# Kernel optimization log

Measured on AMD Instinct MI355X. Metric: run time of the kernel, lower is better.

The kernel has to match this reference:

```python
import jax, jax.numpy as jnp
import numpy as np

MAX_FRAMES = 12
EMBED_DIM = 512
TOPK = 12
NUM_SAMPLES = 500
SIGMA = 0.05
SEL_DIM = 2
NUM_HEADS = 2


def setup_inputs() -> dict:
    key = jax.random.key(0)
    ks = jax.random.split(key, 9)
    D = EMBED_DIM
    C = D // 2
    s = lambda fan_in: 1.0 / np.sqrt(fan_in)
    return {
        "x": jax.random.normal(ks[0], (16, MAX_FRAMES * 50, D), dtype=jnp.float32),
        "ln_g": jnp.ones((D,), jnp.float32),
        "ln_b": jnp.zeros((D,), jnp.float32),
        "w_in": jax.random.normal(ks[1], (D, C), jnp.float32) * s(D),
        "wq": jax.random.normal(ks[2], (C, C), jnp.float32) * s(C),
        "wk": jax.random.normal(ks[3], (C, C), jnp.float32) * s(C),
        "wv": jax.random.normal(ks[4], (C, C), jnp.float32) * s(C),
        "wo": jax.random.normal(ks[5], (C, C), jnp.float32) * s(C),
        "w1": jax.random.normal(ks[6], (2 * C, C), jnp.float32) * s(2 * C),
        "w2": jax.random.normal(ks[7], (C, 1), jnp.float32) * s(C),
    }


def layer_norm(x, g, b, eps=1e-5):
    mu = jnp.mean(x, axis=-1, keepdims=True)
    var = jnp.var(x, axis=-1, keepdims=True)
    return (x - mu) * jax.lax.rsqrt(var + eps) * g + b


def mha(x, wq, wk, wv, wo):
    B, N, C = x.shape
    hd = C // NUM_HEADS
    q = (x @ wq).reshape(B, N, NUM_HEADS, hd).transpose(0, 2, 1, 3)
    k = (x @ wk).reshape(B, N, NUM_HEADS, hd).transpose(0, 2, 1, 3)
    v = (x @ wv).reshape(B, N, NUM_HEADS, hd).transpose(0, 2, 1, 3)
    attn = jax.nn.softmax(jnp.einsum('bhnd,bhmd->bhnm', q, k) / np.sqrt(hd), axis=-1)
    out = jnp.einsum('bhnm,bhmd->bhnd', attn, v).transpose(0, 2, 1, 3).reshape(B, N, C)
    return out @ wo


def predictor(x, ln_g, ln_b, w_in, wq, wk, wv, wo, w1, w2):
    h = jax.nn.gelu(layer_norm(x, ln_g, ln_b) @ w_in, approximate=False)
    h = mha(h, wq, wk, wv, wo)
    B, N, C = h.shape
    g = jnp.mean(h, axis=1, keepdims=True)
    h = jnp.concatenate([h, jnp.broadcast_to(g, (B, N, C))], axis=-1)
    h = jax.nn.gelu(h @ w1, approximate=False)
    return jnp.tanh(h @ w2)  # (B, N, 1)


def perturbed_topk(scores):
    # scores: (b, d) -> soft indicators (b, k, d)
    b, d = scores.shape
    noise = jax.random.normal(jax.random.key(1), (b, NUM_SAMPLES, d), dtype=scores.dtype)
    perturbed = scores[:, None, :] + noise * SIGMA
    _, idx = jax.lax.top_k(perturbed, TOPK)            # (b, ns, k)
    idx = jnp.sort(idx, axis=-1)
    onehot = jax.nn.one_hot(idx, d, dtype=scores.dtype)  # (b, ns, k, d)
    return onehot.mean(axis=1)                          # (b, k, d)


def reference(x, ln_g, ln_b, w_in, wq, wk, wv, wo, w1, w2):
    B, L, D = x.shape
    N = L // MAX_FRAMES
    xf = x.reshape(B * MAX_FRAMES, N, D)
    pred = predictor(xf, ln_g, ln_b, w_in, wq, wk, wv, wo, w1, w2)[..., 0]  # (b, N)
    spatial_score = pred[:, SEL_DIM:]                    # (b, N-2)
    ind = perturbed_topk(spatial_score)                  # (b, k, N-2)
    cls_feat = xf[:, :SEL_DIM, :]
    spatial_feat = xf[:, SEL_DIM:, :]
    sel = jnp.einsum('bkl,bld->bkd', ind, spatial_feat)
    out = jnp.concatenate([cls_feat, sel], axis=1)       # (b, 2+k, D)
    return out.reshape(B, -1, D)
```

## Files before the change

kernel.cpp:

```cpp
#include <hip/hip_runtime.h>
#include <stdint.h>

#define B2      192
#define NTOK    50
#define ROWS    9600
#define D_EMB   512
#define C_DIM   256
#define HD      128
#define NSAMP   500
#define TOPKK   12
#define NSPA    48
#define NSAMP_T 96000
#define NOISE_OFF 61953536ull
#define NOISE_BYTES 18432000ull
#define WS_NEED (NOISE_OFF + NOISE_BYTES)

typedef short short8 __attribute__((ext_vector_type(8)));
typedef float f32x4  __attribute__((ext_vector_type(4)));

__device__ __forceinline__ float gelu_f(float x) {
    return 0.5f * x * (1.0f + erff(x * 0.7071067811865476f));
}
__device__ __forceinline__ uint16_t f2bf(float x) {
    uint32_t u = __float_as_uint(x);
    return (uint16_t)((u + 0x7fffu + ((u >> 16) & 1u)) >> 16);
}
__device__ __forceinline__ float bf2f(uint16_t b) {
    return __uint_as_float(((uint32_t)b) << 16);
}
__device__ __forceinline__ size_t swzA(int m, int k, int K) {
    return ((size_t)(m >> 4) * (K >> 5) + (k >> 5)) * 512
         + (size_t)((((k >> 3) & 3) * 16 + (m & 15)) * 8 + (k & 7));
}

__device__ __forceinline__ uint32_t rotl32(uint32_t x, int r) {
    return (x << r) | (x >> (32 - r));
}
__device__ __forceinline__ void threefry01(uint32_t& x0, uint32_t& x1) {
    const uint32_t ks0 = 0u, ks1 = 1u, ks2 = 0x1BD11BDBu;
    x0 += ks0; x1 += ks1;
#define TFR(r) { x0 += x1; x1 = rotl32(x1, r); x1 ^= x0; }
    TFR(13) TFR(15) TFR(26) TFR(6)  x0 += ks1; x1 += ks2 + 1u;
    TFR(17) TFR(29) TFR(16) TFR(24) x0 += ks2; x1 += ks0 + 2u;
    TFR(13) TFR(15) TFR(26) TFR(6)  x0 += ks0; x1 += ks1 + 3u;
    TFR(17) TFR(29) TFR(16) TFR(24) x0 += ks1; x1 += ks2 + 4u;
    TFR(13) TFR(15) TFR(26) TFR(6)  x0 += ks2; x1 += ks0 + 5u;
#undef TFR
}

__device__ __forceinline__ float erfinv_xla(float x) {
    float w = -log1pf(-x * x);
    float p;
    if (w < 5.0f) {
        w -= 2.5f;
        p = 2.81022636e-08f;
        p = fmaf(p, w, 3.43273939e-07f);
        p = fmaf(p, w, -3.5233877e-06f);
        p = fmaf(p, w, -4.39150654e-06f);
        p = fmaf(p, w, 0.00021858087f);
        p = fmaf(p, w, -0.00125372503f);
        p = fmaf(p, w, -0.00417768164f);
        p = fmaf(p, w, 0.246640727f);
        p = fmaf(p, w, 1.50140941f);
    } else {
        w = sqrtf(w) - 3.0f;
        p = -0.000200214257f;
        p = fmaf(p, w, 0.000100950558f);
        p = fmaf(p, w, 0.00134934322f);
        p = fmaf(p, w, -0.00367342844f);
        p = fmaf(p, w, 0.00573950773f);
        p = fmaf(p, w, -0.0076224613f);
        p = fmaf(p, w, 0.00943887047f);
        p = fmaf(p, w, 1.00167406f);
        p = fmaf(p, w, 2.83297682f);
    }
    return p * x;
}

__device__ __forceinline__ float bits_to_normal(uint32_t bits) {
    float f = __uint_as_float((bits >> 9) | 0x3f800000u) - 1.0f;
    float u = f * 2.0f + (-0.99999994039535522461f);
    u = fmaxf(-0.99999994039535522461f, u);
    return 1.4142135623730951f * erfinv_xla(u);
}

__global__ __launch_bounds__(256) void noise_kernel(float* __restrict__ noise) {
    int T  = blockIdx.x * 256 + threadIdx.x;
    int q  = T / NSAMP_T;
    int g2 = T - q * NSAMP_T;
    uint32_t cbase = (uint32_t)g2 * 48u + (uint32_t)(q * 4);
    float4 o;
    { uint32_t x0=0u, x1=cbase + 0u; threefry01(x0,x1); o.x = bits_to_normal(x0^x1) * 0.05f; }
    { uint32_t x0=0u, x1=cbase + 1u; threefry01(x0,x1); o.y = bits_to_normal(x0^x1) * 0.05f; }
    { uint32_t x0=0u, x1=cbase + 2u; threefry01(x0,x1); o.z = bits_to_normal(x0^x1) * 0.05f; }
    { uint32_t x0=0u, x1=cbase + 3u; threefry01(x0,x1); o.w = bits_to_normal(x0^x1) * 0.05f; }
    ((float4*)noise)[(size_t)q * NSAMP_T + g2] = o;
}

__global__ __launch_bounds__(256) void prep_kernel(const float* __restrict__ x,
                                                   const float* __restrict__ g,
                                                   const float* __restrict__ b,
                                                   short* __restrict__ xh,
                                                   short* __restrict__ xl,
                                                   const float* __restrict__ w_in, const float* __restrict__ wq,
                                                   const float* __restrict__ wk, const float* __restrict__ wv,
                                                   const float* __restrict__ wo, const float* __restrict__ w1,
                                                   short* win_hi, short* win_lo, short* wq_hi, short* wq_lo,
                                                   short* wk_hi, short* wk_lo, short* wv_hi, short* wv_lo,
                                                   short* wo_hi, short* wo_lo, short* w1a_hi, short* w1a_lo) {
    if (blockIdx.x < 2400) {
        int row  = blockIdx.x * 4 + (threadIdx.x >> 6);
        int lane = threadIdx.x & 63;
        const float* rp = x + (size_t)row * D_EMB;
        float4 v0 = *(const float4*)(rp + lane * 8);
        float4 v1 = *(const float4*)(rp + lane * 8 + 4);
        float s  = v0.x + v0.y + v0.z + v0.w + v1.x + v1.y + v1.z + v1.w;
        float s2 = v0.x*v0.x + v0.y*v0.y + v0.z*v0.z + v0.w*v0.w
                 + v1.x*v1.x + v1.y*v1.y + v1.z*v1.z + v1.w*v1.w;
#pragma unroll
        for (int off = 32; off; off >>= 1) {
            s  += __shfl_xor(s,  off);
            s2 += __shfl_xor(s2, off);
        }
        float mu  = s / 512.0f;
        float var = s2 / 512.0f - mu * mu;
        float inv = 1.0f / sqrtf(var + 1e-5f);
        const float* gp = g + lane * 8;
        const float* bp = b + lane * 8;
        float o[8];
        o[0]=(v0.x-mu)*inv*gp[0]+bp[0]; o[1]=(v0.y-mu)*inv*gp[1]+bp[1];
        o[2]=(v0.z-mu)*inv*gp[2]+bp[2]; o[3]=(v0.w-mu)*inv*gp[3]+bp[3];
        o[4]=(v1.x-mu)*inv*gp[4]+bp[4]; o[5]=(v1.y-mu)*inv*gp[5]+bp[5];
        o[6]=(v1.z-mu)*inv*gp[6]+bp[6]; o[7]=(v1.w-mu)*inv*gp[7]+bp[7];
        short8 h8, l8;
#pragma unroll
        for (int j = 0; j < 8; ++j) {
            uint16_t h = f2bf(o[j]);
            h8[j] = (short)h;
            l8[j] = (short)f2bf(o[j] - bf2f(h));
        }
        size_t blk = (size_t)(row >> 4) * 16 + (lane >> 2);
        int inner  = (lane & 3) * 16 + (row & 15);
        ((short8*)xh)[blk * 64 + inner] = h8;
        ((short8*)xl)[blk * 64 + inner] = l8;
    } else {
        int blk = blockIdx.x - 2400;
        const float* W; short *hi, *lo; int K, base;
        if      (blk <  64) { W = w_in; hi = win_hi; lo = win_lo; K = 512; base = 0;   }
        else if (blk <  96) { W = wq;   hi = wq_hi;  lo = wq_lo;  K = 256; base = 64;  }
        else if (blk < 128) { W = wk;   hi = wk_hi;  lo = wk_lo;  K = 256; base = 96;  }
        else if (blk < 160) { W = wv;   hi = wv_hi;  lo = wv_lo;  K = 256; base = 128; }
        else if (blk < 192) { W = wo;   hi = wo_hi;  lo = wo_lo;  K = 256; base = 160; }
        else                { W = w1;   hi = w1a_hi; lo = w1a_lo; K = 256; base = 192; }
        int t = (blk - base) * 256 + threadIdx.x;
        int n = t & 255, k8 = t >> 8;
        short8 h8, l8;
#pragma unroll
        for (int j = 0; j < 8; ++j) {
            float wvl = W[(size_t)(k8 * 8 + j) * 256 + n];
            uint16_t h = f2bf(wvl);
            h8[j] = (short)h;
            l8[j] = (short)f2bf(wvl - bf2f(h));
        }
        size_t bb = (size_t)(n >> 4) * (K >> 5) + (k8 >> 2);
        int inner = (k8 & 3) * 16 + (n & 15);
        ((short8*)hi)[bb * 64 + inner] = h8;
        ((short8*)lo)[bb * 64 + inner] = l8;
    }
}

template<int KB>
__device__ __forceinline__ void mm_core(const short8* __restrict__ pAh, const short8* __restrict__ pAl,
                                        const short8* __restrict__ pBh0, const short8* __restrict__ pBl0,
                                        const short8* __restrict__ pBh1, const short8* __restrict__ pBl1,
                                        f32x4& acc0, f32x4& acc1) {
    short8 ah[3], al[3], bh0[3], bl0[3], bh1[3], bl1[3];
#pragma unroll
    for (int i = 0; i < 2; ++i) {
        int off = i * 64;
        ah[i] = pAh[off];  al[i] = pAl[off];
        bh0[i] = pBh0[off]; bl0[i] = pBl0[off];
        bh1[i] = pBh1[off]; bl1[i] = pBl1[off];
    }
#pragma unroll
    for (int ks = 0; ks < KB; ++ks) {
        int cur = ks % 3;
        if (ks + 2 < KB) {
            int pre = (ks + 2) % 3, off = (ks + 2) * 64;
            ah[pre] = pAh[off];  al[pre] = pAl[off];
            bh0[pre] = pBh0[off]; bl0[pre] = pBl0[off];
            bh1[pre] = pBh1[off]; bl1[pre] = pBl1[off];
        }
        acc0 = __builtin_amdgcn_mfma_f32_16x16x32_bf16(ah[cur], bh0[cur], acc0, 0, 0, 0);
        acc0 = __builtin_amdgcn_mfma_f32_16x16x32_bf16(ah[cur], bl0[cur], acc0, 0, 0, 0);
        acc0 = __builtin_amdgcn_mfma_f32_16x16x32_bf16(al[cur], bh0[cur], acc0, 0, 0, 0);
        acc1 = __builtin_amdgcn_mfma_f32_16x16x32_bf16(ah[cur], bh1[cur], acc1, 0, 0, 0);
        acc1 = __builtin_amdgcn_mfma_f32_16x16x32_bf16(ah[cur], bl1[cur], acc1, 0, 0, 0);
        acc1 = __builtin_amdgcn_mfma_f32_16x16x32_bf16(al[cur], bh1[cur], acc1, 0, 0, 0);
    }
}

__device__ __forceinline__ void epi_store(f32x4 acc, int row0, int col, int N,
                                          float* __restrict__ Cf, short* __restrict__ Chi,
                                          short* __restrict__ Clo,
                                          const float* __restrict__ bias, int act) {
#pragma unroll
    for (int r = 0; r < 4; ++r) {
        int row = row0 + r;
        float v2 = acc[r];
        if (bias) v2 += bias[(size_t)(row / 50) * N + col];
        if (act)  v2 = gelu_f(v2);
        if (Cf) Cf[(size_t)row * N + col] = v2;
        if (Chi) {
            uint16_t h = f2bf(v2);
            size_t ad = swzA(row, col, 256);
            Chi[ad] = (short)h;
            Clo[ad] = (short)f2bf(v2 - bf2f(h));
        }
    }
}

template<int KB>
__global__ __launch_bounds__(256) void gemm_one(const short8* __restrict__ Ah,
                                                const short8* __restrict__ Al,
                                                const short8* __restrict__ Bh,
                                                const short8* __restrict__ Bl,
                                                float* __restrict__ Cf,
                                                short* __restrict__ Chi,
                                                short* __restrict__ Clo,
                                                const float* __restrict__ bias,
                                                int act) {
    int lane = threadIdx.x & 63;
    int wv   = threadIdx.x >> 6;
    int ms   = blockIdx.x * 4 + wv;
    int ns0  = blockIdx.y * 2;
    const short8* pAh  = Ah + (size_t)ms  * KB * 64 + lane;
    const short8* pAl  = Al + (size_t)ms  * KB * 64 + lane;
    const short8* pBh0 = Bh + (size_t)ns0 * KB * 64 + lane;
    const short8* pBl0 = Bl + (size_t)ns0 * KB * 64 + lane;
    const short8* pBh1 = pBh0 + (size_t)KB * 64;
    const short8* pBl1 = pBl0 + (size_t)KB * 64;
    f32x4 acc0 = {0.f,0.f,0.f,0.f}, acc1 = {0.f,0.f,0.f,0.f};
    mm_core<KB>(pAh, pAl, pBh0, pBl0, pBh1, pBl1, acc0, acc1);
    int row0 = ms * 16 + (lane >> 4) * 4;
    int cin  = lane & 15;
    epi_store(acc0, row0, ns0 * 16 + cin,      256, Cf, Chi, Clo, bias, act);
    epi_store(acc1, row0, (ns0 + 1) * 16 + cin, 256, Cf, Chi, Clo, bias, act);
}

__global__ __launch_bounds__(256) void gemm8_pred(const short8* __restrict__ Ah,
                                                  const short8* __restrict__ Al,
                                                  const short8* __restrict__ Bh,
                                                  const short8* __restrict__ Bl,
                                                  const float* __restrict__ gwb,
                                                  const float* __restrict__ w2,
                                                  float* __restrict__ pred_raw) {
    int lane = threadIdx.x & 63;
    int wv   = threadIdx.x >> 6;
    int ms   = blockIdx.x * 4 + wv;
    int ns0  = blockIdx.y * 2;
    const short8* pAh  = Ah + (size_t)ms  * 8 * 64 + lane;
    const short8* pAl  = Al + (size_t)ms  * 8 * 64 + lane;
    const short8* pBh0 = Bh + (size_t)ns0 * 8 * 64 + lane;
    const short8* pBl0 = Bl + (size_t)ns0 * 8 * 64 + lane;
    const short8* pBh1 = pBh0 + 8 * 64;
    const short8* pBl1 = pBl0 + 8 * 64;
    f32x4 acc0 = {0.f,0.f,0.f,0.f}, acc1 = {0.f,0.f,0.f,0.f};
    mm_core<8>(pAh, pAl, pBh0, pBl0, pBh1, pBl1, acc0, acc1);
    int row0 = ms * 16 + (lane >> 4) * 4;
    int cin  = lane & 15;
    int c0   = ns0 * 16 + cin;
    int c1   = (ns0 + 1) * 16 + cin;
    float w2a = w2[c0], w2b = w2[c1];
#pragma unroll
    for (int r = 0; r < 4; ++r) {
        int row = row0 + r;
        int bb  = row / 50;
        float v0 = gelu_f(acc0[r] + gwb[(size_t)bb * 256 + c0]);
        float v1 = gelu_f(acc1[r] + gwb[(size_t)bb * 256 + c1]);
        float t  = v0 * w2a + v1 * w2b;
        t += __shfl_xor(t, 1); t += __shfl_xor(t, 2);
        t += __shfl_xor(t, 4); t += __shfl_xor(t, 8);
        if (cin == 0) atomicAdd(&pred_raw[row], t);
    }
}

__global__ __launch_bounds__(256) void gemm_qkv(const short8* __restrict__ Ah,
                                                const short8* __restrict__ Al,
                                                const short8* __restrict__ Bhq, const short8* __restrict__ Blq,
                                                const short8* __restrict__ Bhk, const short8* __restrict__ Blk,
                                                const short8* __restrict__ Bhv, const short8* __restrict__ Blv,
                                                float* __restrict__ q, float* __restrict__ k,
                                                float* __restrict__ v) {
    int lane = threadIdx.x & 63;
    int wv   = threadIdx.x >> 6;
    int ms   = blockIdx.x * 4 + wv;
    int sel  = blockIdx.y >> 3;
    int ns0  = (blockIdx.y & 7) * 2;
    const short8* Bh = (sel == 0) ? Bhq : (sel == 1) ? Bhk : Bhv;
    const short8* Bl = (sel == 0) ? Blq : (sel == 1) ? Blk : Blv;
    float* C = (sel == 0) ? q : (sel == 1) ? k : v;
    const short8* pAh  = Ah + (size_t)ms  * 8 * 64 + lane;
    const short8* pAl  = Al + (size_t)ms  * 8 * 64 + lane;
    const short8* pBh0 = Bh + (size_t)ns0 * 8 * 64 + lane;
    const short8* pBl0 = Bl + (size_t)ns0 * 8 * 64 + lane;
    const short8* pBh1 = pBh0 + 8 * 64;
    const short8* pBl1 = pBl0 + 8 * 64;
    f32x4 acc0 = {0.f,0.f,0.f,0.f}, acc1 = {0.f,0.f,0.f,0.f};
    mm_core<8>(pAh, pAl, pBh0, pBl0, pBh1, pBl1, acc0, acc1);
    int row0 = ms * 16 + (lane >> 4) * 4;
    int cin  = lane & 15;
    epi_store(acc0, row0, ns0 * 16 + cin,      256, C, nullptr, nullptr, nullptr, 0);
    epi_store(acc1, row0, (ns0 + 1) * 16 + cin, 256, C, nullptr, nullptr, nullptr, 0);
}

#define ASLOT(r, s) ((r) * 128 + (((s) ^ (((r) >> 2) & 7)) << 2))
__global__ __launch_bounds__(256) void attn_kernel(const float* __restrict__ q,
                                                   const float* __restrict__ k,
                                                   const float* __restrict__ v,
                                                   short* __restrict__ aoh,
                                                   short* __restrict__ aol) {
    __shared__ float sQ[NTOK * 128];
    __shared__ float sK[NTOK * 128];
    __shared__ float sS[NTOK * 51];
    int blk = blockIdx.x;
    int b = blk >> 1, h = blk & 1;
    const size_t base = (size_t)b * NTOK * C_DIM + h * HD;
    int tid = threadIdx.x;
    for (int idx = tid; idx < 1600; idx += 256) {
        int r = idx >> 5, s = idx & 31;
        int ps = ASLOT(r, s);
        *(float4*)&sQ[ps] = *(const float4*)(q + base + (size_t)r * C_DIM + s * 4);
        *(float4*)&sK[ps] = *(const float4*)(k + base + (size_t)r * C_DIM + s * 4);
    }
    __syncthreads();
    if (tid < 169) {
        int i2 = tid / 13, j2 = tid - i2 * 13;
        int i0 = i2 * 4, j0 = j2 * 4;
        int kq = i2 & 7, kk = j2 & 7;
        const float* qp[4];
        const float* kp[4];
#pragma unroll
        for (int r = 0; r < 4; ++r) {
            int ir = i0 + r; if (ir > 49) ir = 49;
            int jr = j0 + r; if (jr > 49) jr = 49;
            qp[r] = &sQ[ir * 128];
            kp[r] = &sK[jr * 128];
        }
        f32x4 acc[4][4];
#pragma unroll
        for (int r = 0; r < 4; ++r)
#pragma unroll
            for (int c = 0; c < 4; ++c) acc[r][c] = (f32x4){0.f, 0.f, 0.f, 0.f};
#pragma unroll 4
        for (int t = 0; t < 32; ++t) {
            int oq = (t ^ kq) << 2, ok = (t ^ kk) << 2;
            f32x4 qr[4], kr[4];
#pragma unroll
            for (int r = 0; r < 4; ++r) qr[r] = *(const f32x4*)(qp[r] + oq);
#pragma unroll
            for (int c = 0; c < 4; ++c) kr[c] = *(const f32x4*)(kp[c] + ok);
#pragma unroll
            for (int r = 0; r < 4; ++r)
#pragma unroll
                for (int c = 0; c < 4; ++c) acc[r][c] += qr[r] * kr[c];
        }
        const float sc = 0.08838834764831845f;
#pragma unroll
        for (int r = 0; r < 4; ++r) {
            if (i0 + r < 50) {
#pragma unroll
                for (int c = 0; c < 4; ++c) {
                    if (j0 + c < 50) {
                        f32x4 a = acc[r][c];
                        sS[(i0 + r) * 51 + (j0 + c)] = (a[0] + a[1] + a[2] + a[3]) * sc;
                    }
                }
            }
        }
    }
    __syncthreads();
    for (int idx = tid; idx < 1600; idx += 256) {
        int r = idx >> 5, s = idx & 31;
        *(float4*)&sQ[ASLOT(r, s)] = *(const float4*)(v + base + (size_t)r * C_DIM + s * 4);
    }
    {
        int wid = tid >> 6, lane = tid & 63;
        for (int i = wid; i < NTOK; i += 4) {
            float val = (lane < NTOK) ? sS[i * 51 + lane] : -3.0e38f;
            float m = val;
#pragma unroll
            for (int off = 32; off; off >>= 1) m = fmaxf(m, __shfl_xor(m, off));
            float e2 = expf(val - m);
            float s = e2;
#pragma unroll
            for (int off = 32; off; off >>= 1) s += __shfl_xor(s, off);
            if (lane < NTOK) sS[i * 51 + lane] = e2 * (1.0f / s);
        }
    }
    __syncthreads();
    for (int e = tid; e < 416; e += 256) {
        int i2 = e >> 5;
        int s4 = e & 31;
        int i0 = i2 * 4;
        const float* sr[4];
#pragma unroll
        for (int r = 0; r < 4; ++r) {
            int ir = i0 + r; if (ir > 49) ir = 49;
            sr[r] = &sS[ir * 51];
        }
        f32x4 acc[4];
#pragma unroll
        for (int r = 0; r < 4; ++r) acc[r] = (f32x4){0.f, 0.f, 0.f, 0.f};
        for (int j = 0; j < NTOK; ++j) {
            f32x4 v4 = *(const f32x4*)&sQ[ASLOT(j, s4)];
#pragma unroll
            for (int r = 0; r < 4; ++r) acc[r] += v4 * sr[r][j];
        }
#pragma unroll
        for (int r = 0; r < 4; ++r) {
            if (i0 + r < 50) {
                int row = b * NTOK + i0 + r;
#pragma unroll
                for (int c = 0; c < 4; ++c) {
                    int col = h * HD + s4 * 4 + c;
                    float val = acc[r][c];
                    uint16_t hh2 = f2bf(val);
                    size_t ad = swzA(row, col, 256);
                    aoh[ad] = (short)hh2;
                    aol[ad] = (short)f2bf(val - bf2f(hh2));
                }
            }
        }
    }
}
#undef ASLOT

__global__ __launch_bounds__(256) void mean_gw(const float* __restrict__ h2,
                                               const float* __restrict__ w1,
                                               float* __restrict__ gw) {
    __shared__ float sg[C_DIM];
    int b = blockIdx.x, d = threadIdx.x;
    float s = 0.f;
    for (int n = 0; n < NTOK; ++n) s += h2[((size_t)b * NTOK + n) * C_DIM + d];
    sg[d] = s * 0.02f;
    __syncthreads();
    const float* wb = w1 + 256 * 256;
    float acc = 0.f;
#pragma unroll 4
    for (int k = 0; k < C_DIM; ++k)
        acc = fmaf(sg[k], wb[(size_t)k * 256 + d], acc);
    gw[(size_t)b * C_DIM + d] = acc;
}

__device__ __forceinline__ unsigned long long topk_key(uint32_t base, int d,
                                                       const float* __restrict__ sp) {
    uint32_t x0 = 0u, x1 = base + (uint32_t)d;
    threefry01(x0, x1);
    float n  = bits_to_normal(x0 ^ x1);
    float v  = tanhf(sp[d]) + n * 0.05f;
    uint32_t vb   = __float_as_uint(v);
    uint32_t mono = (vb & 0x80000000u) ? ~vb : (vb | 0x80000000u);
    return ((unsigned long long)mono << 6) | (unsigned)(63 - d);
}

#define STEP(li) { unsigned long long mn_ = (key < li) ? key : li; \
                   li = (key > li) ? key : li; key = mn_; }
#define S1  STEP(l0)
#define S2  S1  STEP(l1)
#define S3  S2  STEP(l2)
#define S4  S3  STEP(l3)
#define S5  S4  STEP(l4)
#define S6  S5  STEP(l5)
#define S7  S6  STEP(l6)
#define S8  S7  STEP(l7)
#define S9  S8  STEP(l8)
#define S10 S9  STEP(l9)
#define S11 S10 STEP(l10)
#define S12 S11 STEP(l11)

#define TOPK_MERGE_TAIL                                                        \
    int rowL = p * 64 + lane;                                                  \
    if (hh == 1) {                                                             \
        unsigned long long* r = sK[rowL];                                      \
        r[0]=l0; r[1]=l1; r[2]=l2;  r[3]=l3;  r[4]=l4;   r[5]=l5;              \
        r[6]=l6; r[7]=l7; r[8]=l8;  r[9]=l9;  r[10]=l10; r[11]=l11;            \
    }                                                                          \
    __syncthreads();                                                           \
    if (hh == 0) {                                                             \
        const unsigned long long* r = sK[rowL];                                \
        unsigned long long M0  = (l0  > r[11]) ? l0  : r[11];                  \
        unsigned long long M1  = (l1  > r[10]) ? l1  : r[10];                  \
        unsigned long long M2  = (l2  > r[9])  ? l2  : r[9];                   \
        unsigned long long M3  = (l3  > r[8])  ? l3  : r[8];                   \
        unsigned long long M4  = (l4  > r[7])  ? l4  : r[7];                   \
        unsigned long long M5  = (l5  > r[6])  ? l5  : r[6];                   \
        unsigned long long M6  = (l6  > r[5])  ? l6  : r[5];                   \
        unsigned long long M7  = (l7  > r[4])  ? l7  : r[4];                   \
        unsigned long long M8  = (l8  > r[3])  ? l8  : r[3];                   \
        unsigned long long M9  = (l9  > r[2])  ? l9  : r[2];                   \
        unsigned long long M10 = (l10 > r[1])  ? l10 : r[1];                   \
        unsigned long long M11 = (l11 > r[0])  ? l11 : r[0];                   \
        unsigned long long m = 0ull;                                           \
        m |= 1ull << (unsigned)(M0  & 63ull);  m |= 1ull << (unsigned)(M1  & 63ull); \
        m |= 1ull << (unsigned)(M2  & 63ull);  m |= 1ull << (unsigned)(M3  & 63ull); \
        m |= 1ull << (unsigned)(M4  & 63ull);  m |= 1ull << (unsigned)(M5  & 63ull); \
        m |= 1ull << (unsigned)(M6  & 63ull);  m |= 1ull << (unsigned)(M7  & 63ull); \
        m |= 1ull << (unsigned)(M8  & 63ull);  m |= 1ull << (unsigned)(M9  & 63ull); \
        m |= 1ull << (unsigned)(M10 & 63ull);  m |= 1ull << (unsigned)(M11 & 63ull); \
        EMIT(M0)  EMIT(M1)  EMIT(M2)  EMIT(M3)  EMIT(M4)  EMIT(M5)             \
        EMIT(M6)  EMIT(M7)  EMIT(M8)  EMIT(M9)  EMIT(M10) EMIT(M11)            \
    }
#define EMIT(Mi) { unsigned a_ = (unsigned)(Mi & 63ull); \
                   int kpos_ = 11 - __popcll(m & ((1ull << a_) - 1ull)); \
                   int d_ = 63 - (int)a_; \
                   atomicAdd(&counts[((size_t)b * TOPKK + kpos_) * NSPA + d_], 1); }

__global__ __launch_bounds__(256, 4) void topk_noise(const float* __restrict__ pred,
                                                     const float4* __restrict__ nz4,
                                                     int* __restrict__ counts) {
    __shared__ unsigned long long sK[128][13];
    __shared__ float sSP[2][48];
    int lane = threadIdx.x & 63;
    int wv   = threadIdx.x >> 6;
    int p    = wv >> 1;
    int hh   = wv & 1;
    int b0   = (blockIdx.x * 128) / NSAMP;
    if (threadIdx.x < 96) {
        int r = threadIdx.x / 48, dd = threadIdx.x - r * 48;
        int bb = b0 + r; if (bb > B2 - 1) bb = B2 - 1;
        sSP[r][dd] = tanhf(pred[bb * NTOK + 2 + dd]);
    }
    int g = blockIdx.x * 128 + p * 64 + lane;
    int b = g / NSAMP;
    int bo = b - b0;
    __syncthreads();
    const float* spl = &sSP[bo][hh * 24];
    const float4* nq = nz4 + (size_t)(hh * 6) * NSAMP_T + g;

    float4 n0 = nq[0 * NSAMP_T], n1 = nq[1 * NSAMP_T], n2 = nq[2 * NSAMP_T];
    float4 n3 = nq[3 * NSAMP_T], n4 = nq[4 * NSAMP_T], n5 = nq[5 * NSAMP_T];

    unsigned long long l0=0ull,l1=0ull,l2=0ull,l3=0ull,l4=0ull,l5=0ull,
                       l6=0ull,l7=0ull,l8=0ull,l9=0ull,l10=0ull,l11=0ull;
    unsigned long long key;

#define MKKEY(dd, nv) { float v_ = spl[dd] + (nv); uint32_t vb_ = __float_as_uint(v_); \
    uint32_t mono_ = (vb_ & 0x80000000u) ? ~vb_ : (vb_ | 0x80000000u); \
    key = ((unsigned long long)mono_ << 6) | (unsigned)(63 - (hh * 24 + (dd))); }

    MKKEY(0,  n0.x) S1   MKKEY(1,  n0.y) S2   MKKEY(2,  n0.z) S3   MKKEY(3,  n0.w) S4
    MKKEY(4,  n1.x) S5   MKKEY(5,  n1.y) S6   MKKEY(6,  n1.z) S7   MKKEY(7,  n1.w) S8
    MKKEY(8,  n2.x) S9   MKKEY(9,  n2.y) S10  MKKEY(10, n2.z) S11  MKKEY(11, n2.w) S12
    MKKEY(12, n3.x) S12  MKKEY(13, n3.y) S12  MKKEY(14, n3.z) S12  MKKEY(15, n3.w) S12
    MKKEY(16, n4.x) S12  MKKEY(17, n4.y) S12  MKKEY(18, n4.z) S12  MKKEY(19, n4.w) S12
    MKKEY(20, n5.x) S12  MKKEY(21, n5.y) S12  MKKEY(22, n5.z) S12  MKKEY(23, n5.w) S12
#undef MKKEY

    TOPK_MERGE_TAIL
}

__global__ __launch_bounds__(256, 4) void topk_fb(const float* __restrict__ pred,
                                                  int* __restrict__ counts) {
    __shared__ unsigned long long sK[128][13];
    int lane = threadIdx.x & 63;
    int wv   = threadIdx.x >> 6;
    int p    = wv >> 1;
    int hh   = wv & 1;
    int g    = blockIdx.x * 128 + p * 64 + lane;
    int b    = g / NSAMP;
    int s    = g - b * NSAMP;
    uint32_t base = (uint32_t)((b * NSAMP + s) * NSPA);
    const float* sp = pred + b * NTOK + 2;
    int d0 = hh * 24;

    unsigned long long l0=0ull,l1=0ull,l2=0ull,l3=0ull,l4=0ull,l5=0ull,
                       l6=0ull,l7=0ull,l8=0ull,l9=0ull,l10=0ull,l11=0ull;
    unsigned long long key;

    key = topk_key(base, d0 + 0,  sp); S1
    key = topk_key(base, d0 + 1,  sp); S2
    key = topk_key(base, d0 + 2,  sp); S3
    key = topk_key(base, d0 + 3,  sp); S4
    key = topk_key(base, d0 + 4,  sp); S5
    key = topk_key(base, d0 + 5,  sp); S6
    key = topk_key(base, d0 + 6,  sp); S7
    key = topk_key(base, d0 + 7,  sp); S8
    key = topk_key(base, d0 + 8,  sp); S9
    key = topk_key(base, d0 + 9,  sp); S10
    key = topk_key(base, d0 + 10, sp); S11
    key = topk_key(base, d0 + 11, sp); S12
#pragma unroll 2
    for (int dd = 12; dd < 24; ++dd) {
        key = topk_key(base, d0 + dd, sp); S12
    }

    TOPK_MERGE_TAIL
}
#undef EMIT
#undef TOPK_MERGE_TAIL
#undef STEP
#undef S1
#undef S2
#undef S3
#undef S4
#undef S5
#undef S6
#undef S7
#undef S8
#undef S9
#undef S10
#undef S11
#undef S12

__global__ __launch_bounds__(256) void select_out2(const float* __restrict__ x,
                                                   const int* __restrict__ counts,
                                                   float* __restrict__ out) {
    int b = blockIdx.x;
    int d = threadIdx.x;
    __shared__ float sw[TOPKK * NSPA];
    __shared__ int anyl[NSPA];
    for (int i = d; i < TOPKK * NSPA; i += 256)
        sw[i] = (float)counts[(size_t)b * TOPKK * NSPA + i] * 0.002f;
    __syncthreads();
    if (d < NSPA) {
        int a = 0;
        for (int k2 = 0; k2 < TOPKK; ++k2) a |= (sw[k2 * NSPA + d] != 0.0f);
        anyl[d] = a;
    }
    __syncthreads();
    {
        const float* xr0 = x + (size_t)(b * NTOK) * D_EMB;
        out[(size_t)(b * 14 + 0) * D_EMB + d]       = xr0[d];
        out[(size_t)(b * 14 + 0) * D_EMB + d + 256] = xr0[d + 256];
        out[(size_t)(b * 14 + 1) * D_EMB + d]       = xr0[D_EMB + d];
        out[(size_t)(b * 14 + 1) * D_EMB + d + 256] = xr0[D_EMB + d + 256];
    }
    float a0[TOPKK], a1[TOPKK];
#pragma unroll
    for (int k2 = 0; k2 < TOPKK; ++k2) { a0[k2] = 0.f; a1[k2] = 0.f; }
    for (int l = 0; l < NSPA; ++l) {
        if (!anyl[l]) continue;
        const float* xr = x + (size_t)(b * NTOK + 2 + l) * D_EMB;
        float v0 = xr[d], v1 = xr[d + 256];
#pragma unroll
        for (int k2 = 0; k2 < TOPKK; ++k2) {
            float w = sw[k2 * NSPA + l];
            a0[k2] = fmaf(w, v0, a0[k2]);
            a1[k2] = fmaf(w, v1, a1[k2]);
        }
    }
#pragma unroll
    for (int k2 = 0; k2 < TOPKK; ++k2) {
        out[(size_t)(b * 14 + 2 + k2) * D_EMB + d]       = a0[k2];
        out[(size_t)(b * 14 + 2 + k2) * D_EMB + d + 256] = a1[k2];
    }
}

extern "C" void kernel_launch(void* const* d_in, const int* in_sizes, int n_in,
                              void* d_out, int out_size, void* d_ws, size_t ws_size,
                              hipStream_t stream) {
    const float* x    = (const float*)d_in[0];
    const float* ln_g = (const float*)d_in[1];
    const float* ln_b = (const float*)d_in[2];
    const float* w_in = (const float*)d_in[3];
    const float* wq   = (const float*)d_in[4];
    const float* wk   = (const float*)d_in[5];
    const float* wv   = (const float*)d_in[6];
    const float* wo   = (const float*)d_in[7];
    const float* w1   = (const float*)d_in[8];
    const float* w2   = (const float*)d_in[9];
    float* out = (float*)d_out;

    char* W = (char*)d_ws;
    short* xn_hi  = (short*)(W + 0);
    short* xn_lo  = (short*)(W + 9830400);
    short* ao_hi  = (short*)(W + 0);
    short* ao_lo  = (short*)(W + 4915200);
    short* h2_hi  = (short*)(W + 9830400);
    short* h2_lo  = (short*)(W + 14745600);
    short* h1_hi  = (short*)(W + 19660800);
    short* h1_lo  = (short*)(W + 24576000);
    float* q      = (float*)(W + 29491200);
    float* h2f    = (float*)(W + 29491200);
    float* k      = (float*)(W + 39321600);
    float* v      = (float*)(W + 49152000);
    short* win_hi = (short*)(W + 58982400);
    short* win_lo = (short*)(W + 59244544);
    short* wq_hi  = (short*)(W + 59506688);
    short* wq_lo  = (short*)(W + 59637760);
    short* wk_hi  = (short*)(W + 59768832);
    short* wk_lo  = (short*)(W + 59899904);
    short* wv_hi  = (short*)(W + 60030976);
    short* wv_lo  = (short*)(W + 60162048);
    short* wo_hi  = (short*)(W + 60293120);
    short* wo_lo  = (short*)(W + 60424192);
    short* w1a_hi = (short*)(W + 60555264);
    short* w1a_lo = (short*)(W + 60686336);
    float* gw     = (float*)(W + 61276160);
    float* pred   = (float*)(W + 61472768);
    int*   counts = (int*)  (W + 61511168);
    float* noise  = (float*)(W + NOISE_OFF);

    const bool nzmode = ws_size >= WS_NEED;

    hipMemsetAsync(W + 61472768, 0, 38400 + (size_t)B2 * TOPKK * NSPA * sizeof(int), stream);
    if (nzmode) noise_kernel<<<4500, 256, 0, stream>>>(noise);
    prep_kernel<<<2624, 256, 0, stream>>>(x, ln_g, ln_b, xn_hi, xn_lo,
        w_in, wq, wk, wv, wo, w1,
        win_hi, win_lo, wq_hi, wq_lo, wk_hi, wk_lo, wv_hi, wv_lo,
        wo_hi, wo_lo, w1a_hi, w1a_lo);
    gemm_one<16><<<dim3(150, 8), 256, 0, stream>>>((const short8*)xn_hi, (const short8*)xn_lo,
        (const short8*)win_hi, (const short8*)win_lo, nullptr, h1_hi, h1_lo, nullptr, 1);
    gemm_qkv<<<dim3(150, 24), 256, 0, stream>>>((const short8*)h1_hi, (const short8*)h1_lo,
        (const short8*)wq_hi, (const short8*)wq_lo, (const short8*)wk_hi, (const short8*)wk_lo,
        (const short8*)wv_hi, (const short8*)wv_lo, q, k, v);
    attn_kernel<<<B2 * 2, 256, 0, stream>>>(q, k, v, ao_hi, ao_lo);
    gemm_one<8><<<dim3(150, 8), 256, 0, stream>>>((const short8*)ao_hi, (const short8*)ao_lo,
        (const short8*)wo_hi, (const short8*)wo_lo, h2f, h2_hi, h2_lo, nullptr, 0);
    mean_gw<<<B2, 256, 0, stream>>>(h2f, w1, gw);
    gemm8_pred<<<dim3(150, 8), 256, 0, stream>>>((const short8*)h2_hi, (const short8*)h2_lo,
        (const short8*)w1a_hi, (const short8*)w1a_lo, gw, w2, pred);
    if (nzmode) topk_noise<<<750, 256, 0, stream>>>(pred, (const float4*)noise, counts);
    else        topk_fb<<<750, 256, 0, stream>>>(pred, counts);
    select_out2<<<B2, 256, 0, stream>>>(x, counts, out);
}
```

Baseline: 299.0 us.

## Fuse perturbed top-k with output selection into one per-batch kernel

Merges the top-k sampling and the selection kernel into one kernel with one 1024-thread block per frame. Counts are accumulated with shared-memory atomics instead of global atomics. The memset is removed, and zeroing of pred moves into mean_gw. This cuts a launch, the global count traffic and the memset, but the grid drops to 192 large blocks and uses more LDS per block, so occupancy may be lower.

```diff
diff --git a/kernel.cpp b/kernel.cpp
--- a/kernel.cpp
+++ b/kernel.cpp
@@ -438,9 +438,11 @@
 
 __global__ __launch_bounds__(256) void mean_gw(const float* __restrict__ h2,
                                                const float* __restrict__ w1,
-                                               float* __restrict__ gw) {
+                                               float* __restrict__ gw,
+                                               float* __restrict__ pred_raw) {
     __shared__ float sg[C_DIM];
     int b = blockIdx.x, d = threadIdx.x;
+    if (d < NTOK) pred_raw[b * NTOK + d] = 0.0f;
     float s = 0.f;
     for (int n = 0; n < NTOK; ++n) s += h2[((size_t)b * NTOK + n) * C_DIM + d];
     sg[d] = s * 0.02f;
@@ -451,17 +453,6 @@
     for (int k = 0; k < C_DIM; ++k)
         acc = fmaf(sg[k], wb[(size_t)k * 256 + d], acc);
     gw[(size_t)b * C_DIM + d] = acc;
-}
-
-__device__ __forceinline__ unsigned long long topk_key(uint32_t base, int d,
-                                                       const float* __restrict__ sp) {
-    uint32_t x0 = 0u, x1 = base + (uint32_t)d;
-    threefry01(x0, x1);
-    float n  = bits_to_normal(x0 ^ x1);
-    float v  = tanhf(sp[d]) + n * 0.05f;
-    uint32_t vb   = __float_as_uint(v);
-    uint32_t mono = (vb & 0x80000000u) ? ~vb : (vb | 0x80000000u);
-    return ((unsigned long long)mono << 6) | (unsigned)(63 - d);
 }
 
 #define STEP(li) { unsigned long long mn_ = (key < li) ? key : li; \
@@ -479,126 +470,128 @@
 #define S11 S10 STEP(l10)
 #define S12 S11 STEP(l11)
 
-#define TOPK_MERGE_TAIL                                                        \
-    int rowL = p * 64 + lane;                                                  \
-    if (hh == 1) {                                                             \
-        unsigned long long* r = sK[rowL];                                      \
-        r[0]=l0; r[1]=l1; r[2]=l2;  r[3]=l3;  r[4]=l4;   r[5]=l5;              \
-        r[6]=l6; r[7]=l7; r[8]=l8;  r[9]=l9;  r[10]=l10; r[11]=l11;            \
-    }                                                                          \
-    __syncthreads();                                                           \
-    if (hh == 0) {                                                             \
-        const unsigned long long* r = sK[rowL];                                \
-        unsigned long long M0  = (l0  > r[11]) ? l0  : r[11];                  \
-        unsigned long long M1  = (l1  > r[10]) ? l1  : r[10];                  \
-        unsigned long long M2  = (l2  > r[9])  ? l2  : r[9];                   \
-        unsigned long long M3  = (l3  > r[8])  ? l3  : r[8];                   \
-        unsigned long long M4  = (l4  > r[7])  ? l4  : r[7];                   \
-        unsigned long long M5  = (l5  > r[6])  ? l5  : r[6];                   \
-        unsigned long long M6  = (l6  > r[5])  ? l6  : r[5];                   \
-        unsigned long long M7  = (l7  > r[4])  ? l7  : r[4];                   \
-        unsigned long long M8  = (l8  > r[3])  ? l8  : r[3];                   \
-        unsigned long long M9  = (l9  > r[2])  ? l9  : r[2];                   \
-        unsigned long long M10 = (l10 > r[1])  ? l10 : r[1];                   \
-        unsigned long long M11 = (l11 > r[0])  ? l11 : r[0];                   \
-        unsigned long long m = 0ull;                                           \
-        m |= 1ull << (unsigned)(M0  & 63ull);  m |= 1ull << (unsigned)(M1  & 63ull); \
-        m |= 1ull << (unsigned)(M2  & 63ull);  m |= 1ull << (unsigned)(M3  & 63ull); \
-        m |= 1ull << (unsigned)(M4  & 63ull);  m |= 1ull << (unsigned)(M5  & 63ull); \
-        m |= 1ull << (unsigned)(M6  & 63ull);  m |= 1ull << (unsigned)(M7  & 63ull); \
-        m |= 1ull << (unsigned)(M8  & 63ull);  m |= 1ull << (unsigned)(M9  & 63ull); \
-        m |= 1ull << (unsigned)(M10 & 63ull);  m |= 1ull << (unsigned)(M11 & 63ull); \
-        EMIT(M0)  EMIT(M1)  EMIT(M2)  EMIT(M3)  EMIT(M4)  EMIT(M5)             \
-        EMIT(M6)  EMIT(M7)  EMIT(M8)  EMIT(M9)  EMIT(M10) EMIT(M11)            \
-    }
+template<int NZ>
+__global__ __launch_bounds__(1024, 4) void topk_select(const float* __restrict__ pred,
+                                                       const float4* __restrict__ nz4,
+                                                       const float* __restrict__ x,
+                                                       float* __restrict__ out) {
+    __shared__ unsigned long long sK[500][13];
+    __shared__ int scnt[TOPKK * NSPA];
+    __shared__ float sSP[NSPA];
+    __shared__ int anyl[NSPA];
+    int b   = blockIdx.x;
+    int tid = threadIdx.x;
+    int hh  = tid >> 9;
+    int s   = tid & 511;
+    for (int i = tid; i < TOPKK * NSPA; i += 1024) scnt[i] = 0;
+    if (tid < NSPA) sSP[tid] = tanhf(pred[b * NTOK + 2 + tid]);
+    __syncthreads();
+    bool act = (s < NSAMP);
+
+    unsigned long long l0=0ull,l1=0ull,l2=0ull,l3=0ull,l4=0ull,l5=0ull,
+                       l6=0ull,l7=0ull,l8=0ull,l9=0ull,l10=0ull,l11=0ull;
+    unsigned long long key;
+    if (act) {
+        if (NZ) {
+            const float* spl = &sSP[hh * 24];
+            int g = b * NSAMP + s;
+            const float4* nq = nz4 + (size_t)(hh * 6) * NSAMP_T + g;
+            float4 n0 = nq[0 * NSAMP_T], n1 = nq[1 * NSAMP_T], n2 = nq[2 * NSAMP_T];
+            float4 n3 = nq[3 * NSAMP_T], n4 = nq[4 * NSAMP_T], n5 = nq[5 * NSAMP_T];
+#define MKKEY(dd, nv) { float v_ = spl[dd] + (nv); uint32_t vb_ = __float_as_uint(v_); \
+    uint32_t mono_ = (vb_ & 0x80000000u) ? ~vb_ : (vb_ | 0x80000000u); \
+    key = ((unsigned long long)mono_ << 6) | (unsigned)(63 - (hh * 24 + (dd))); }
+            MKKEY(0,  n0.x) S1   MKKEY(1,  n0.y) S2   MKKEY(2,  n0.z) S3   MKKEY(3,  n0.w) S4
+            MKKEY(4,  n1.x) S5   MKKEY(5,  n1.y) S6   MKKEY(6,  n1.z) S7   MKKEY(7,  n1.w) S8
+            MKKEY(8,  n2.x) S9   MKKEY(9,  n2.y) S10  MKKEY(10, n2.z) S11  MKKEY(11, n2.w) S12
+            MKKEY(12, n3.x) S12  MKKEY(13, n3.y) S12  MKKEY(14, n3.z) S12  MKKEY(15, n3.w) S12
+            MKKEY(16, n4.x) S12  MKKEY(17, n4.y) S12  MKKEY(18, n4.z) S12  MKKEY(19, n4.w) S12
+            MKKEY(20, n5.x) S12  MKKEY(21, n5.y) S12  MKKEY(22, n5.z) S12  MKKEY(23, n5.w) S12
+#undef MKKEY
+        } else {
+            uint32_t base = (uint32_t)((b * NSAMP + s) * NSPA);
+            int d0 = hh * 24;
+#define FBKEY(dd) { int d_ = d0 + (dd); uint32_t x0_ = 0u, x1_ = base + (uint32_t)d_; \
+    threefry01(x0_, x1_); float v_ = sSP[d_] + bits_to_normal(x0_ ^ x1_) * 0.05f; \
+    uint32_t vb_ = __float_as_uint(v_); \
+    uint32_t mono_ = (vb_ & 0x80000000u) ? ~vb_ : (vb_ | 0x80000000u); \
+    key = ((unsigned long long)mono_ << 6) | (unsigned)(63 - d_); }
+            FBKEY(0)  S1   FBKEY(1)  S2   FBKEY(2)  S3   FBKEY(3)  S4
+            FBKEY(4)  S5   FBKEY(5)  S6   FBKEY(6)  S7   FBKEY(7)  S8
+            FBKEY(8)  S9   FBKEY(9)  S10  FBKEY(10) S11  FBKEY(11) S12
+#pragma unroll 2
+            for (int dd = 12; dd < 24; ++dd) { FBKEY(dd) S12 }
+#undef FBKEY
+        }
+        if (hh == 1) {
+            unsigned long long* r = sK[s];
+            r[0]=l0; r[1]=l1; r[2]=l2;  r[3]=l3;  r[4]=l4;   r[5]=l5;
+            r[6]=l6; r[7]=l7; r[8]=l8;  r[9]=l9;  r[10]=l10; r[11]=l11;
+        }
+    }
+    __syncthreads();
+    if (act && hh == 0) {
+        const unsigned long long* r = sK[s];
+        unsigned long long M0  = (l0  > r[11]) ? l0  : r[11];
+        unsigned long long M1  = (l1  > r[10]) ? l1  : r[10];
+        unsigned long long M2  = (l2  > r[9])  ? l2  : r[9];
+        unsigned long long M3  = (l3  > r[8])  ? l3  : r[8];
+        unsigned long long M4  = (l4  > r[7])  ? l4  : r[7];
+        unsigned long long M5  = (l5  > r[6])  ? l5  : r[6];
+        unsigned long long M6  = (l6  > r[5])  ? l6  : r[5];
+        unsigned long long M7  = (l7  > r[4])  ? l7  : r[4];
+        unsigned long long M8  = (l8  > r[3])  ? l8  : r[3];
+        unsigned long long M9  = (l9  > r[2])  ? l9  : r[2];
+        unsigned long long M10 = (l10 > r[1])  ? l10 : r[1];
+        unsigned long long M11 = (l11 > r[0])  ? l11 : r[0];
+        unsigned long long m = 0ull;
+        m |= 1ull << (unsigned)(M0  & 63ull);  m |= 1ull << (unsigned)(M1  & 63ull);
+        m |= 1ull << (unsigned)(M2  & 63ull);  m |= 1ull << (unsigned)(M3  & 63ull);
+        m |= 1ull << (unsigned)(M4  & 63ull);  m |= 1ull << (unsigned)(M5  & 63ull);
+        m |= 1ull << (unsigned)(M6  & 63ull);  m |= 1ull << (unsigned)(M7  & 63ull);
+        m |= 1ull << (unsigned)(M8  & 63ull);  m |= 1ull << (unsigned)(M9  & 63ull);
+        m |= 1ull << (unsigned)(M10 & 63ull);  m |= 1ull << (unsigned)(M11 & 63ull);
 #define EMIT(Mi) { unsigned a_ = (unsigned)(Mi & 63ull); \
                    int kpos_ = 11 - __popcll(m & ((1ull << a_) - 1ull)); \
                    int d_ = 63 - (int)a_; \
-                   atomicAdd(&counts[((size_t)b * TOPKK + kpos_) * NSPA + d_], 1); }
-
-__global__ __launch_bounds__(256, 4) void topk_noise(const float* __restrict__ pred,
-                                                     const float4* __restrict__ nz4,
-                                                     int* __restrict__ counts) {
-    __shared__ unsigned long long sK[128][13];
-    __shared__ float sSP[2][48];
-    int lane = threadIdx.x & 63;
-    int wv   = threadIdx.x >> 6;
-    int p    = wv >> 1;
-    int hh   = wv & 1;
-    int b0   = (blockIdx.x * 128) / NSAMP;
-    if (threadIdx.x < 96) {
-        int r = threadIdx.x / 48, dd = threadIdx.x - r * 48;
-        int bb = b0 + r; if (bb > B2 - 1) bb = B2 - 1;
-        sSP[r][dd] = tanhf(pred[bb * NTOK + 2 + dd]);
-    }
-    int g = blockIdx.x * 128 + p * 64 + lane;
-    int b = g / NSAMP;
-    int bo = b - b0;
-    __syncthreads();
-    const float* spl = &sSP[bo][hh * 24];
-    const float4* nq = nz4 + (size_t)(hh * 6) * NSAMP_T + g;
-
-    float4 n0 = nq[0 * NSAMP_T], n1 = nq[1 * NSAMP_T], n2 = nq[2 * NSAMP_T];
-    float4 n3 = nq[3 * NSAMP_T], n4 = nq[4 * NSAMP_T], n5 = nq[5 * NSAMP_T];
-
-    unsigned long long l0=0ull,l1=0ull,l2=0ull,l3=0ull,l4=0ull,l5=0ull,
-                       l6=0ull,l7=0ull,l8=0ull,l9=0ull,l10=0ull,l11=0ull;
-    unsigned long long key;
-
-#define MKKEY(dd, nv) { float v_ = spl[dd] + (nv); uint32_t vb_ = __float_as_uint(v_); \
-    uint32_t mono_ = (vb_ & 0x80000000u) ? ~vb_ : (vb_ | 0x80000000u); \
-    key = ((unsigned long long)mono_ << 6) | (unsigned)(63 - (hh * 24 + (dd))); }
-
-    MKKEY(0,  n0.x) S1   MKKEY(1,  n0.y) S2   MKKEY(2,  n0.z) S3   MKKEY(3,  n0.w) S4
-    MKKEY(4,  n1.x) S5   MKKEY(5,  n1.y) S6   MKKEY(6,  n1.z) S7   MKKEY(7,  n1.w) S8
-    MKKEY(8,  n2.x) S9   MKKEY(9,  n2.y) S10  MKKEY(10, n2.z) S11  MKKEY(11, n2.w) S12
-    MKKEY(12, n3.x) S12  MKKEY(13, n3.y) S12  MKKEY(14, n3.z) S12  MKKEY(15, n3.w) S12
-    MKKEY(16, n4.x) S12  MKKEY(17, n4.y) S12  MKKEY(18, n4.z) S12  MKKEY(19, n4.w) S12
-    MKKEY(20, n5.x) S12  MKKEY(21, n5.y) S12  MKKEY(22, n5.z) S12  MKKEY(23, n5.w) S12
-#undef MKKEY
-
-    TOPK_MERGE_TAIL
-}
-
-__global__ __launch_bounds__(256, 4) void topk_fb(const float* __restrict__ pred,
-                                                  int* __restrict__ counts) {
-    __shared__ unsigned long long sK[128][13];
-    int lane = threadIdx.x & 63;
-    int wv   = threadIdx.x >> 6;
-    int p    = wv >> 1;
-    int hh   = wv & 1;
-    int g    = blockIdx.x * 128 + p * 64 + lane;
-    int b    = g / NSAMP;
-    int s    = g - b * NSAMP;
-    uint32_t base = (uint32_t)((b * NSAMP + s) * NSPA);
-    const float* sp = pred + b * NTOK + 2;
-    int d0 = hh * 24;
-
-    unsigned long long l0=0ull,l1=0ull,l2=0ull,l3=0ull,l4=0ull,l5=0ull,
-                       l6=0ull,l7=0ull,l8=0ull,l9=0ull,l10=0ull,l11=0ull;
-    unsigned long long key;
-
-    key = topk_key(base, d0 + 0,  sp); S1
-    key = topk_key(base, d0 + 1,  sp); S2
-    key = topk_key(base, d0 + 2,  sp); S3
-    key = topk_key(base, d0 + 3,  sp); S4
-    key = topk_key(base, d0 + 4,  sp); S5
-    key = topk_key(base, d0 + 5,  sp); S6
-    key = topk_key(base, d0 + 6,  sp); S7
-    key = topk_key(base, d0 + 7,  sp); S8
-    key = topk_key(base, d0 + 8,  sp); S9
-    key = topk_key(base, d0 + 9,  sp); S10
-    key = topk_key(base, d0 + 10, sp); S11
-    key = topk_key(base, d0 + 11, sp); S12
-#pragma unroll 2
-    for (int dd = 12; dd < 24; ++dd) {
-        key = topk_key(base, d0 + dd, sp); S12
-    }
-
-    TOPK_MERGE_TAIL
-}
+                   atomicAdd(&scnt[kpos_ * NSPA + d_], 1); }
+        EMIT(M0)  EMIT(M1)  EMIT(M2)  EMIT(M3)  EMIT(M4)  EMIT(M5)
+        EMIT(M6)  EMIT(M7)  EMIT(M8)  EMIT(M9)  EMIT(M10) EMIT(M11)
 #undef EMIT
-#undef TOPK_MERGE_TAIL
+    }
+    __syncthreads();
+    if (tid < NSPA) {
+        int a = 0;
+#pragma unroll
+        for (int k2 = 0; k2 < TOPKK; ++k2) a |= scnt[k2 * NSPA + tid];
+        anyl[tid] = a;
+    }
+    __syncthreads();
+    if (hh == 0) {
+        const float* xr0 = x + (size_t)(b * NTOK) * D_EMB;
+        out[(size_t)(b * 14 + 0) * D_EMB + s] = xr0[s];
+        out[(size_t)(b * 14 + 1) * D_EMB + s] = xr0[D_EMB + s];
+    }
+    float a0, a1, a2, a3, a4, a5;
+    a0 = a1 = a2 = a3 = a4 = a5 = 0.f;
+    int k0 = hh * 6;
+    for (int l = 0; l < NSPA; ++l) {
+        if (!anyl[l]) continue;
+        float v = x[((size_t)(b * NTOK + 2 + l)) * D_EMB + s];
+        a0 = fmaf((float)scnt[(k0 + 0) * NSPA + l] * 0.002f, v, a0);
+        a1 = fmaf((float)scnt[(k0 + 1) * NSPA + l] * 0.002f, v, a1);
+        a2 = fmaf((float)scnt[(k0 + 2) * NSPA + l] * 0.002f, v, a2);
+        a3 = fmaf((float)scnt[(k0 + 3) * NSPA + l] * 0.002f, v, a3);
+        a4 = fmaf((float)scnt[(k0 + 4) * NSPA + l] * 0.002f, v, a4);
+        a5 = fmaf((float)scnt[(k0 + 5) * NSPA + l] * 0.002f, v, a5);
+    }
+    out[(size_t)(b * 14 + 2 + k0 + 0) * D_EMB + s] = a0;
+    out[(size_t)(b * 14 + 2 + k0 + 1) * D_EMB + s] = a1;
+    out[(size_t)(b * 14 + 2 + k0 + 2) * D_EMB + s] = a2;
+    out[(size_t)(b * 14 + 2 + k0 + 3) * D_EMB + s] = a3;
+    out[(size_t)(b * 14 + 2 + k0 + 4) * D_EMB + s] = a4;
+    out[(size_t)(b * 14 + 2 + k0 + 5) * D_EMB + s] = a5;
+}
 #undef STEP
 #undef S1
 #undef S2
@@ -612,50 +605,6 @@
 #undef S10
 #undef S11
 #undef S12
-
-__global__ __launch_bounds__(256) void select_out2(const float* __restrict__ x,
-                                                   const int* __restrict__ counts,
-                                                   float* __restrict__ out) {
-    int b = blockIdx.x;
-    int d = threadIdx.x;
-    __shared__ float sw[TOPKK * NSPA];
-    __shared__ int anyl[NSPA];
-    for (int i = d; i < TOPKK * NSPA; i += 256)
-        sw[i] = (float)counts[(size_t)b * TOPKK * NSPA + i] * 0.002f;
-    __syncthreads();
-    if (d < NSPA) {
-        int a = 0;
-        for (int k2 = 0; k2 < TOPKK; ++k2) a |= (sw[k2 * NSPA + d] != 0.0f);
-        anyl[d] = a;
-    }
-    __syncthreads();
-    {
-        const float* xr0 = x + (size_t)(b * NTOK) * D_EMB;
-        out[(size_t)(b * 14 + 0) * D_EMB + d]       = xr0[d];
-        out[(size_t)(b * 14 + 0) * D_EMB + d + 256] = xr0[d + 256];
-        out[(size_t)(b * 14 + 1) * D_EMB + d]       = xr0[D_EMB + d];
-        out[(size_t)(b * 14 + 1) * D_EMB + d + 256] = xr0[D_EMB + d + 256];
-    }
-    float a0[TOPKK], a1[TOPKK];
-#pragma unroll
-    for (int k2 = 0; k2 < TOPKK; ++k2) { a0[k2] = 0.f; a1[k2] = 0.f; }
-    for (int l = 0; l < NSPA; ++l) {
-        if (!anyl[l]) continue;
-        const float* xr = x + (size_t)(b * NTOK + 2 + l) * D_EMB;
-        float v0 = xr[d], v1 = xr[d + 256];
-#pragma unroll
-        for (int k2 = 0; k2 < TOPKK; ++k2) {
-            float w = sw[k2 * NSPA + l];
-            a0[k2] = fmaf(w, v0, a0[k2]);
-            a1[k2] = fmaf(w, v1, a1[k2]);
-        }
-    }
-#pragma unroll
-    for (int k2 = 0; k2 < TOPKK; ++k2) {
-        out[(size_t)(b * 14 + 2 + k2) * D_EMB + d]       = a0[k2];
-        out[(size_t)(b * 14 + 2 + k2) * D_EMB + d + 256] = a1[k2];
-    }
-}
 
 extern "C" void kernel_launch(void* const* d_in, const int* in_sizes, int n_in,
                               void* d_out, int out_size, void* d_ws, size_t ws_size,
@@ -699,12 +648,10 @@
     short* w1a_lo = (short*)(W + 60686336);
     float* gw     = (float*)(W + 61276160);
     float* pred   = (float*)(W + 61472768);
-    int*   counts = (int*)  (W + 61511168);
     float* noise  = (float*)(W + NOISE_OFF);
 
     const bool nzmode = ws_size >= WS_NEED;
 
-    hipMemsetAsync(W + 61472768, 0, 38400 + (size_t)B2 * TOPKK * NSPA * sizeof(int), stream);
     if (nzmode) noise_kernel<<<4500, 256, 0, stream>>>(noise);
     prep_kernel<<<2624, 256, 0, stream>>>(x, ln_g, ln_b, xn_hi, xn_lo,
         w_in, wq, wk, wv, wo, w1,
@@ -718,10 +665,9 @@
     attn_kernel<<<B2 * 2, 256, 0, stream>>>(q, k, v, ao_hi, ao_lo);
     gemm_one<8><<<dim3(150, 8), 256, 0, stream>>>((const short8*)ao_hi, (const short8*)ao_lo,
         (const short8*)wo_hi, (const short8*)wo_lo, h2f, h2_hi, h2_lo, nullptr, 0);
-    mean_gw<<<B2, 256, 0, stream>>>(h2f, w1, gw);
+    mean_gw<<<B2, 256, 0, stream>>>(h2f, w1, gw, pred);
     gemm8_pred<<<dim3(150, 8), 256, 0, stream>>>((const short8*)h2_hi, (const short8*)h2_lo,
         (const short8*)w1a_hi, (const short8*)w1a_lo, gw, w2, pred);
-    if (nzmode) topk_noise<<<750, 256, 0, stream>>>(pred, (const float4*)noise, counts);
-    else        topk_fb<<<750, 256, 0, stream>>>(pred, counts);
-    select_out2<<<B2, 256, 0, stream>>>(x, counts, out);
-}
+    if (nzmode) topk_select<1><<<B2, 1024, 0, stream>>>(pred, (const float4*)noise, x, out);
+    else        topk_select<0><<<B2, 1024, 0, stream>>>(pred, nullptr, x, out);
+}
```

Result: faster. 275.5 us (-7.8%).
